# Kernel tuning notes

Measured on AMD Instinct MI355X. Metric: run time of the kernel, lower is better.

Reference implementation:

```python
import jax, jax.numpy as jnp
import numpy as np

# ---- dims ----
V, VR, E, H, NF = 100000, 5000, 300, 256, 150
H2 = 2 * H  # 512


def _lstm_dir(x, Wih, Whh, b, h0, c0):
    # x: (T, B, E); returns hs (T, B, H), final (h, c)
    def step(carry, xt):
        h, c = carry
        z = xt @ Wih.T + h @ Whh.T + b
        i, f, g, o = jnp.split(z, 4, axis=-1)  # torch gate order i,f,g,o
        c = jax.nn.sigmoid(f) * c + jax.nn.sigmoid(i) * jnp.tanh(g)
        h = jax.nn.sigmoid(o) * jnp.tanh(c)
        return (h, c), h
    (hT, cT), hs = jax.lax.scan(step, (h0, c0), x)
    return hs, hT, cT


def bilstm(x, Wih_f, Whh_f, b_f, Wih_b, Whh_b, b_b, state=None):
    # x: (T, B, E) -> out (T, B, 2H), state tuple
    B = x.shape[1]
    if state is None:
        z = jnp.zeros((B, H), x.dtype)
        state = (z, z, z, z)
    h0f, c0f, h0b, c0b = state
    hs_f, hTf, cTf = _lstm_dir(x, Wih_f, Whh_f, b_f, h0f, c0f)
    hs_b, hTb, cTb = _lstm_dir(x[::-1], Wih_b, Whh_b, b_b, h0b, c0b)
    out = jnp.concatenate([hs_f, hs_b[::-1]], axis=-1)
    return out, (hTf, cTf, hTb, cTb)


def abwim_atten(question_out, word_rel, rela_rel, word_emb, rela_emb,
                Wih_f, Whh_f, b_f, Wih_b, Whh_b, b_b, W):
    # question_out: (B, 2H, Sq); word_rel (B,Sw), rela_rel (B,Sr) int
    rela = rela_emb[rela_rel.T]   # (Sr, B, E)
    word = word_emb[word_rel.T]   # (Sw, B, E)
    word_out, state = bilstm(word, Wih_f, Whh_f, b_f, Wih_b, Whh_b, b_b)
    rela_out, _ = bilstm(rela, Wih_f, Whh_f, b_f, Wih_b, Whh_b, b_b, state)
    relation = jnp.concatenate([rela_out, word_out], axis=0).transpose(1, 0, 2)  # (B, R, 2H)
    energy = jnp.einsum('brh,hk,bks->brs', relation, W, question_out)  # (B, R, Sq)
    B, R, Sq = energy.shape
    scale = 1.0 / np.sqrt(R).astype(np.float32)
    alpha = jax.nn.softmax(energy.reshape(B, R * Sq) * scale, axis=-1).reshape(B, R, Sq)
    # sum_r alpha[b,r,s] * relation[b,r,h] -> (B, 2H, Sq)
    return jnp.einsum('brs,brh->bhs', alpha, relation)


def setup_inputs():
    key = jax.random.key(0)
    ks = jax.random.split(key, 24)
    B, Sq, Sw, Sr = 64, 40, 12, 4
    s_emb, s_lstm, s_w = 0.05, 0.05, 0.04
    inp = {
        'question': jax.random.randint(ks[0], (B, Sq), 0, V),
        'word_relation': jax.random.randint(ks[1], (B, Sw), 0, V),
        'rela_relation': jax.random.randint(ks[2], (B, Sr), 0, VR),
        'word_previous': jax.random.randint(ks[3], (B, Sw), 0, V),
        'rela_previous': jax.random.randint(ks[4], (B, Sr), 0, VR),
        'word_emb': jax.random.normal(ks[5], (V, E), jnp.float32) * s_emb,
        'rela_emb': jax.random.normal(ks[6], (VR, E), jnp.float32) * s_emb,
        'Wih_f': jax.random.normal(ks[7], (4 * H, E), jnp.float32) * s_lstm,
        'Whh_f': jax.random.normal(ks[8], (4 * H, H), jnp.float32) * s_lstm,
        'b_f': jnp.zeros((4 * H,), jnp.float32),
        'Wih_b': jax.random.normal(ks[9], (4 * H, E), jnp.float32) * s_lstm,
        'Whh_b': jax.random.normal(ks[10], (4 * H, H), jnp.float32) * s_lstm,
        'b_b': jnp.zeros((4 * H,), jnp.float32),
        'W': jax.random.normal(ks[11], (H2, H2), jnp.float32) * s_w,
        'cnn1_w': jax.random.normal(ks[12], (NF, 2 * H2, 1), jnp.float32) * s_w,
        'cnn1_b': jnp.zeros((NF,), jnp.float32),
        'cnn2_w': jax.random.normal(ks[13], (NF, 2 * H2, 3), jnp.float32) * s_w,
        'cnn2_b': jnp.zeros((NF,), jnp.float32),
        'cnn3_w': jax.random.normal(ks[14], (NF, 2 * H2, 5), jnp.float32) * s_w,
        'cnn3_b': jnp.zeros((NF,), jnp.float32),
        'lin_w': jax.random.normal(ks[15], (1, NF), jnp.float32) * s_w,
        'lin2_w': jax.random.normal(ks[16], (H2, H2), jnp.float32) * s_w,
        'lin2_b': jnp.zeros((H2,), jnp.float32),
    }
    return inp


def _conv1d(x, w, b):
    # x: (B, C, L), w: (O, C, K)
    y = jax.lax.conv_general_dilated(x, w, (1,), 'VALID',
                                     dimension_numbers=('NCH', 'OIH', 'NCH'))
    return y + b[None, :, None]


def reference(question, word_relation, rela_relation, word_previous, rela_previous,
              word_emb, rela_emb, Wih_f, Whh_f, b_f, Wih_b, Whh_b, b_b, W,
              cnn1_w, cnn1_b, cnn2_w, cnn2_b, cnn3_w, cnn3_b, lin_w, lin2_w, lin2_b):
    lstm_p = (Wih_f, Whh_f, b_f, Wih_b, Whh_b, b_b)
    # question encoder (dropout is identity at eval)
    q = word_emb[question.T]                      # (Sq, B, E)
    q_out, _ = bilstm(q, *lstm_p)                 # (Sq, B, 2H)
    question_out = q_out.transpose(1, 2, 0)       # (B, 2H, Sq)
    # reduce one previous hop
    atten_prev = abwim_atten(question_out, word_previous, rela_previous,
                             word_emb, rela_emb, *lstm_p, W)
    qo = question_out - atten_prev
    qo = qo.transpose(0, 2, 1) @ lin2_w.T + lin2_b   # (B, Sq, 2H)
    question_out = qo.transpose(0, 2, 1)             # (B, 2H, Sq)
    # current relation attention
    atten_relation = abwim_atten(question_out, word_relation, rela_relation,
                                 word_emb, rela_emb, *lstm_p, W)
    M = jnp.concatenate([question_out, atten_relation], axis=1)  # (B, 4H, Sq)
    h1 = jnp.max(jax.nn.relu(_conv1d(M, cnn1_w, cnn1_b)), axis=2)  # (B, NF)
    h2 = jnp.max(jax.nn.relu(_conv1d(M, cnn2_w, cnn2_b)), axis=2)
    h3 = jnp.max(jax.nn.relu(_conv1d(M, cnn3_w, cnn3_b)), axis=2)
    h = jnp.maximum(jnp.maximum(h1, h2), h3)
    score = (h @ lin_w.T).squeeze(-1)  # (B,)
    return score
```

## Files before the change

### kernel.cpp

```cpp
#include <hip/hip_runtime.h>
#include <math.h>

#define NEG_INF (-3.402823466e+38f)

typedef __attribute__((ext_vector_type(8))) short short8;
typedef __attribute__((ext_vector_type(8))) unsigned short ushort8;
typedef __attribute__((ext_vector_type(4))) float f32x4;

constexpr int NTOK = 4608;
constexpr int BH = 64 * 256;

constexpr size_t OFF_WQ    = 0;
constexpr size_t OFF_B2    = OFF_WQ    + 524288;
constexpr size_t OFF_XB3T  = OFF_B2    + 2048;
constexpr size_t OFF_WB3T  = OFF_XB3T  + 983040;
constexpr size_t OFF_L2B3T = OFF_WB3T  + 393216;
constexpr size_t OFF_C1B3T = OFF_L2B3T + 393216;
constexpr size_t OFF_C2B3T = OFF_C1B3T + 294912;
constexpr size_t OFF_C3B3T = OFF_C2B3T + 884736;
constexpr size_t OFF_XHI   = OFF_C3B3T + 1474560;
constexpr size_t OFF_XLO   = OFF_XHI   + 737280;
constexpr size_t OFF_XP    = OFF_XLO   + 737280;
constexpr size_t OFF_HSQ   = OFF_XP    + 9437184;
constexpr size_t OFF_HSWP  = OFF_HSQ   + 1310720;
constexpr size_t OFF_HSRP  = OFF_HSWP  + 393216;
constexpr size_t OFF_HSWR  = OFF_HSRP  + 131072;
constexpr size_t OFF_HSRR  = OFF_HSWR  + 393216;
constexpr size_t OFF_CS    = OFF_HSRR  + 131072;
constexpr size_t OFF_RELP  = OFF_CS    + 163840;
constexpr size_t OFF_RELC  = OFF_RELP  + 524288;
constexpr size_t OFF_RELW  = OFF_RELC  + 524288;
constexpr size_t OFF_EN    = OFF_RELW  + 524288;

__device__ inline unsigned short f2bf(float f) {
  unsigned int u = __float_as_uint(f);
  u += 0x7FFFu + ((u >> 16) & 1u);
  return (unsigned short)(u >> 16);
}
__device__ inline float bf2f(unsigned short h) {
  return __uint_as_float(((unsigned int)h) << 16);
}
__device__ inline short8 mk8(unsigned long long a, unsigned long long b) {
  union { unsigned long long q[2]; short8 s; } u;
  u.q[0] = a; u.q[1] = b; return u.s;
}
#define ALD(p) __hip_atomic_load((p), __ATOMIC_RELAXED, __HIP_MEMORY_SCOPE_AGENT)

__global__ __launch_bounds__(256) void k_prep(
    const float* __restrict__ Whh_f, const float* __restrict__ Whh_b,
    const float* __restrict__ b_f,   const float* __restrict__ b_b,
    const float* __restrict__ Wih_f, const float* __restrict__ Wih_b,
    const float* __restrict__ Wat,   const float* __restrict__ l2w,
    const float* __restrict__ c1w, const float* __restrict__ c2w, const float* __restrict__ c3w,
    unsigned short* __restrict__ WHB, float* __restrict__ B2,
    unsigned short* __restrict__ XB3T, unsigned short* __restrict__ WB3T,
    unsigned short* __restrict__ L2B3T,
    unsigned short* __restrict__ C1B3T, unsigned short* __restrict__ C2B3T,
    unsigned short* __restrict__ C3B3T, int* __restrict__ flags) {
  int idx = blockIdx.x * 256 + threadIdx.x;
  if (idx < 3072)
    __hip_atomic_store(flags + idx * 16, 0, __ATOMIC_RELAXED, __HIP_MEMORY_SCOPE_AGENT);
  if (idx < 1048576) {
    int e = idx & 511;
    int k = e & 255, isLo = e >> 8;
    int row = (idx >> 9) & 63;
    int tile = (idx >> 15) & 15;
    int d = idx >> 19;
    int g = row >> 4, uu = row & 15;
    int u = tile * 16 + uu;
    const float* Wh = d ? Whh_b : Whh_f;
    float w = Wh[(size_t)(g * 256 + u) * 256 + k];
    unsigned short hi = f2bf(w);
    WHB[idx] = isLo ? f2bf(w - bf2f(hi)) : hi;
    return;
  }
  idx -= 1048576;
  if (idx < 2048) { B2[idx] = (idx < 1024) ? b_f[idx] : b_b[idx-1024]; return; }
  idx -= 2048;
  unsigned short* dst; int n, k, K;
  float w;
  if (idx < 655360) {
    n = idx / 320; k = idx % 320; K = 320; dst = XB3T;
    w = (k < 300) ? ((n < 1024) ? Wih_f[(size_t)n*300 + k] : Wih_b[(size_t)(n-1024)*300 + k]) : 0.f;
  } else if ((idx -= 655360) < 262144) {
    n = idx >> 9; k = idx & 511; K = 512; dst = WB3T;
    w = Wat[(size_t)k*512 + n];
  } else if ((idx -= 262144) < 262144) {
    n = idx >> 9; k = idx & 511; K = 512; dst = L2B3T;
    w = l2w[(size_t)n*512 + k];
  } else if ((idx -= 262144) < 196608) {
    n = idx >> 10; k = idx & 1023; K = 1024; dst = C1B3T;
    w = (n < 150) ? c1w[(size_t)n*1024 + k] : 0.f;
  } else if ((idx -= 196608) < 589824) {
    n = idx / 3072; k = idx % 3072; K = 3072; dst = C2B3T;
    int kw = k >> 10, c = k & 1023;
    w = (n < 150) ? c2w[((size_t)n*1024 + c)*3 + kw] : 0.f;
  } else if ((idx -= 589824) < 983040) {
    n = idx / 5120; k = idx % 5120; K = 5120; dst = C3B3T;
    int kw = k >> 10, c = k & 1023;
    w = (n < 150) ? c3w[((size_t)n*1024 + c)*5 + kw] : 0.f;
  } else return;
  unsigned short hi = f2bf(w);
  unsigned short lo = f2bf(w - bf2f(hi));
  size_t base = (size_t)n * (3*K);
  dst[base + k] = hi;
  dst[base + K + k] = lo;
  dst[base + 2*K + k] = hi;
}

__global__ __launch_bounds__(320) void k_gather(
    const int* __restrict__ q,  const int* __restrict__ wr, const int* __restrict__ rr,
    const int* __restrict__ wp, const int* __restrict__ rp,
    const float* __restrict__ we, const float* __restrict__ re,
    unsigned short* __restrict__ Xhi, unsigned short* __restrict__ Xlo) {
  int m = blockIdx.x, k = threadIdx.x;
  const float* emb; int row;
  if (m < 2560)      { int t=m>>6,    b=m&63; row = q [b*40+t]; emb = we; }
  else if (m < 3328) { int mm=m-2560; int t=mm>>6,b=mm&63; row = wp[b*12+t]; emb = we; }
  else if (m < 3584) { int mm=m-3328; int t=mm>>6,b=mm&63; row = rp[b*4 +t]; emb = re; }
  else if (m < 4352) { int mm=m-3584; int t=mm>>6,b=mm&63; row = wr[b*12+t]; emb = we; }
  else               { int mm=m-4352; int t=mm>>6,b=mm&63; row = rr[b*4 +t]; emb = re; }
  float v = (k < 300) ? emb[(size_t)row*300 + k] : 0.f;
  unsigned short hi = f2bf(v);
  Xhi[(size_t)m*320 + k] = hi;
  Xlo[(size_t)m*320 + k] = f2bf(v - bf2f(hi));
}

template<bool BIAS>
__global__ __launch_bounds__(256) void k_mgemm(
    const unsigned short* __restrict__ Ahi, const unsigned short* __restrict__ Alo, int lda,
    const unsigned short* __restrict__ Bt, const float* __restrict__ bias,
    float* __restrict__ C, int N, int K) {
  __shared__ unsigned short As[64 * 40];
  __shared__ unsigned short Bs[64 * 40];
  int tid = threadIdx.x;
  int wave = tid >> 6, lane = tid & 63;
  int quad = lane >> 4, l16 = lane & 15;
  int m0 = blockIdx.x << 6, n0 = blockIdx.y << 6;
  int K3 = 3 * K;
  int sr = tid >> 2;
  int sc = (tid & 3) << 3;
  f32x4 acc[4] = {};
  for (int k0 = 0; k0 < K3; k0 += 32) {
    int c = (k0 >= K) + (k0 >= 2*K);
    const unsigned short* Asrc = (c == 2) ? Alo : Ahi;
    int kk = k0 - c * K;
    ushort8 av = *(const ushort8*)(Asrc + (size_t)(m0 + sr) * lda + kk + sc);
    ushort8 bv = *(const ushort8*)(Bt + (size_t)(n0 + sr) * K3 + k0 + sc);
    *(ushort8*)&As[sr * 40 + sc] = av;
    *(ushort8*)&Bs[sr * 40 + sc] = bv;
    __syncthreads();
    short8 a  = *(const short8*)&As[(wave*16 + l16) * 40 + quad*8];
    short8 b0 = *(const short8*)&Bs[( 0 + l16) * 40 + quad*8];
    short8 b1 = *(const short8*)&Bs[(16 + l16) * 40 + quad*8];
    short8 b2 = *(const short8*)&Bs[(32 + l16) * 40 + quad*8];
    short8 b3 = *(const short8*)&Bs[(48 + l16) * 40 + quad*8];
    acc[0] = __builtin_amdgcn_mfma_f32_16x16x32_bf16(a, b0, acc[0], 0, 0, 0);
    acc[1] = __builtin_amdgcn_mfma_f32_16x16x32_bf16(a, b1, acc[1], 0, 0, 0);
    acc[2] = __builtin_amdgcn_mfma_f32_16x16x32_bf16(a, b2, acc[2], 0, 0, 0);
    acc[3] = __builtin_amdgcn_mfma_f32_16x16x32_bf16(a, b3, acc[3], 0, 0, 0);
    __syncthreads();
  }
  int row0 = m0 + wave * 16 + quad * 4;
#pragma unroll
  for (int t = 0; t < 4; t++) {
    int col = n0 + t * 16 + l16;
    float bb = BIAS ? bias[col] : 0.f;
#pragma unroll
    for (int r = 0; r < 4; r++)
      C[(size_t)(row0 + r) * N + col] = acc[t][r] + bb;
  }
}

__global__ __launch_bounds__(256) void k_cgemm(
    const unsigned short* __restrict__ Ahi, const unsigned short* __restrict__ Alo,
    const unsigned short* __restrict__ B1, const unsigned short* __restrict__ B2c,
    const unsigned short* __restrict__ B3,
    float* __restrict__ Y1, float* __restrict__ Y2, float* __restrict__ Y3) {
  __shared__ unsigned short As[64 * 40];
  __shared__ unsigned short Bs[64 * 40];
  int z = blockIdx.z;
  const unsigned short* Bt; float* Y; int K, sidx, chunk;
  if (z < 4)       { Bt = B1;  Y = Y1; K = 1024; sidx = z;      chunk = 768;  }
  else if (z < 12) { Bt = B2c; Y = Y2; K = 3072; sidx = z - 4;  chunk = 1152; }
  else             { Bt = B3;  Y = Y3; K = 5120; sidx = z - 12; chunk = 1920; }
  int K3 = 3 * K;
  int ks = sidx * chunk, ke = ks + chunk;
  int tid = threadIdx.x;
  int wave = tid >> 6, lane = tid & 63;
  int quad = lane >> 4, l16 = lane & 15;
  int m0 = blockIdx.x << 6, n0 = blockIdx.y << 6;
  int sr = tid >> 2;
  int sc = (tid & 3) << 3;
  f32x4 acc[4] = {};
  for (int k0 = ks; k0 < ke; k0 += 32) {
    int c = (k0 >= K) + (k0 >= 2*K);
    const unsigned short* Asrc = (c == 2) ? Alo : Ahi;
    int kk = k0 - c * K;
    ushort8 av = *(const ushort8*)(Asrc + (size_t)(m0 + sr) * 1024 + kk + sc);
    ushort8 bv = *(const ushort8*)(Bt + (size_t)(n0 + sr) * K3 + k0 + sc);
    *(ushort8*)&As[sr * 40 + sc] = av;
    *(ushort8*)&Bs[sr * 40 + sc] = bv;
    __syncthreads();
    short8 a  = *(const short8*)&As[(wave*16 + l16) * 40 + quad*8];
    short8 b0 = *(const short8*)&Bs[( 0 + l16) * 40 + quad*8];
    short8 b1 = *(const short8*)&Bs[(16 + l16) * 40 + quad*8];
    short8 b2 = *(const short8*)&Bs[(32 + l16) * 40 + quad*8];
    short8 b3 = *(const short8*)&Bs[(48 + l16) * 40 + quad*8];
    acc[0] = __builtin_amdgcn_mfma_f32_16x16x32_bf16(a, b0, acc[0], 0, 0, 0);
    acc[1] = __builtin_amdgcn_mfma_f32_16x16x32_bf16(a, b1, acc[1], 0, 0, 0);
    acc[2] = __builtin_amdgcn_mfma_f32_16x16x32_bf16(a, b2, acc[2], 0, 0, 0);
    acc[3] = __builtin_amdgcn_mfma_f32_16x16x32_bf16(a, b3, acc[3], 0, 0, 0);
    __syncthreads();
  }
  int row0 = m0 + wave * 16 + quad * 4;
#pragma unroll
  for (int t = 0; t < 4; t++) {
    int col = n0 + t * 16 + l16;
#pragma unroll
    for (int r = 0; r < 4; r++)
      atomicAdd(&Y[(size_t)(row0 + r) * 192 + col], acc[t][r]);
  }
}

__global__ __launch_bounds__(256) void k_zero(float* __restrict__ p, int n4) {
  int idx = blockIdx.x * 256 + threadIdx.x;
  if (idx < n4) *(float4*)(p + (size_t)idx * 4) = make_float4(0.f, 0.f, 0.f, 0.f);
}

__global__ __launch_bounds__(256, 1) void k_steps(
    const unsigned short* __restrict__ WHB, const float* __restrict__ XP,
    float* __restrict__ hsQ, float* __restrict__ hsWp, float* __restrict__ hsRp,
    float* __restrict__ hsWr, float* __restrict__ hsRr,
    unsigned short* __restrict__ Hhi, unsigned short* __restrict__ Hlo,
    int* __restrict__ flags) {
  int bid = blockIdx.x;
  int chain = bid & 7;
  if (chain >= 6) return;
  int tile = bid >> 3;
  int dir = chain & 1, fam = chain >> 1;
  int tid = threadIdx.x;
  int wave = tid >> 6, lane = tid & 63;
  int quad = lane >> 4, l16 = lane & 15;
  int u0 = tile << 4;

  const unsigned short* wsrc = WHB + (((size_t)dir * 16 + tile) << 15);
  short8 Bh[4][8], Bl[4][8];
#pragma unroll
  for (int nf = 0; nf < 4; nf++)
#pragma unroll
    for (int j = 0; j < 8; j++) {
      const unsigned short* wr = wsrc + (nf * 16 + l16) * 512 + j * 32 + quad * 8;
      Bh[nf][j] = *(const short8*)(wr);
      Bl[nf][j] = *(const short8*)(wr + 256);
    }

  int nsteps = (fam == 0) ? 40 : 16;
  float creg[4] = {0.f, 0.f, 0.f, 0.f};
  int row64 = (wave * 16 + l16) * 64 + quad * 2;

  for (int cs = 0; cs < nsteps; cs++) {
    int t, T, seg; float* hsb;
    if (fam == 0)     { t = cs;      T = 40; seg = 0;                         hsb = hsQ + (size_t)dir * 40 * BH; }
    else if (cs < 12) { t = cs;      T = 12; seg = (fam == 1) ? 2560 : 3584;  hsb = ((fam == 1) ? hsWp : hsWr) + (size_t)dir * 12 * BH; }
    else              { t = cs - 12; T = 4;  seg = (fam == 1) ? 3328 : 4352;  hsb = ((fam == 1) ? hsRp : hsRr) + (size_t)dir * 4 * BH; }
    int t_in = dir ? (T - 1 - t) : t;
    int u = u0 + l16;
    const float* xb = XP + (size_t)(seg + t_in * 64) * 2048 + dir * 1024 + u;
    float xi[4], xf[4], xg[4], xo[4];
#pragma unroll
    for (int r = 0; r < 4; r++) {
      const float* xr = xb + (size_t)(wave * 16 + quad * 4 + r) * 2048;
      xi[r] = xr[0]; xf[r] = xr[256]; xg[r] = xr[512]; xo[r] = xr[768];
    }

    f32x4 acc[4] = {};
    if (cs > 0) {
      if (tid < 16) {
        const int* fp = flags + ((((chain << 1) | ((cs - 1) & 1)) * 16 + tid) << 4);
        while (__hip_atomic_load(fp, __ATOMIC_RELAXED, __HIP_MEMORY_SCOPE_AGENT) < cs)
          __builtin_amdgcn_s_sleep(2);
      }
      __syncthreads();
      size_t slotq = (size_t)(chain * 2 + ((cs - 1) & 1)) * 4096;
      const unsigned long long* ph = (const unsigned long long*)Hhi + slotq + row64;
      const unsigned long long* pl = (const unsigned long long*)Hlo + slotq + row64;
      unsigned long long rv[32];
#pragma unroll
      for (int j = 0; j < 8; j++) { rv[2*j] = ALD(ph + 8*j); rv[2*j+1] = ALD(ph + 8*j + 1); }
#pragma unroll
      for (int j = 0; j < 8; j++) { rv[16+2*j] = ALD(pl + 8*j); rv[16+2*j+1] = ALD(pl + 8*j + 1); }
      short8 ah[8], al[8];
#pragma unroll
      for (int j = 0; j < 8; j++) { ah[j] = mk8(rv[2*j], rv[2*j+1]); al[j] = mk8(rv[16+2*j], rv[16+2*j+1]); }
#pragma unroll
      for (int j = 0; j < 8; j++) {
        acc[0] = __builtin_amdgcn_mfma_f32_16x16x32_bf16(ah[j], Bh[0][j], acc[0], 0, 0, 0);
        acc[1] = __builtin_amdgcn_mfma_f32_16x16x32_bf16(ah[j], Bh[1][j], acc[1], 0, 0, 0);
        acc[2] = __builtin_amdgcn_mfma_f32_16x16x32_bf16(ah[j], Bh[2][j], acc[2], 0, 0, 0);
        acc[3] = __builtin_amdgcn_mfma_f32_16x16x32_bf16(ah[j], Bh[3][j], acc[3], 0, 0, 0);
      }
#pragma unroll
      for (int j = 0; j < 8; j++) {
        acc[0] = __builtin_amdgcn_mfma_f32_16x16x32_bf16(ah[j], Bl[0][j], acc[0], 0, 0, 0);
        acc[1] = __builtin_amdgcn_mfma_f32_16x16x32_bf16(ah[j], Bl[1][j], acc[1], 0, 0, 0);
        acc[2] = __builtin_amdgcn_mfma_f32_16x16x32_bf16(ah[j], Bl[2][j], acc[2], 0, 0, 0);
        acc[3] = __builtin_amdgcn_mfma_f32_16x16x32_bf16(ah[j], Bl[3][j], acc[3], 0, 0, 0);
      }
#pragma unroll
      for (int j = 0; j < 8; j++) {
        acc[0] = __builtin_amdgcn_mfma_f32_16x16x32_bf16(al[j], Bh[0][j], acc[0], 0, 0, 0);
        acc[1] = __builtin_amdgcn_mfma_f32_16x16x32_bf16(al[j], Bh[1][j], acc[1], 0, 0, 0);
        acc[2] = __builtin_amdgcn_mfma_f32_16x16x32_bf16(al[j], Bh[2][j], acc[2], 0, 0, 0);
        acc[3] = __builtin_amdgcn_mfma_f32_16x16x32_bf16(al[j], Bh[3][j], acc[3], 0, 0, 0);
      }
    }
    float hnv[4];
#pragma unroll
    for (int r = 0; r < 4; r++) {
      float zi = acc[0][r] + xi[r];
      float zf = acc[1][r] + xf[r];
      float zg = acc[2][r] + xg[r];
      float zo = acc[3][r] + xo[r];
      float gi = 1.f / (1.f + expf(-zi));
      float gf = 1.f / (1.f + expf(-zf));
      float go = 1.f / (1.f + expf(-zo));
      float gg = tanhf(zg);
      float cn = gf * creg[r] + gi * gg;
      hnv[r] = go * tanhf(cn);
      creg[r] = cn;
    }
    size_t oslot = (size_t)(chain * 2 + (cs & 1)) << 14;
    unsigned short* oh = Hhi + oslot;
    unsigned short* ol = Hlo + oslot;
#pragma unroll
    for (int r = 0; r < 4; r++) {
      int b = wave * 16 + quad * 4 + r;
      unsigned short h16 = f2bf(hnv[r]);
      unsigned short l16v = f2bf(hnv[r] - bf2f(h16));
      unsigned int pk = (unsigned int)h16 | ((unsigned int)l16v << 16);
      unsigned int pw = (unsigned int)__shfl_xor((int)pk, 1, 64);
      if ((lane & 1) == 0) {
        unsigned int hw = (pk & 0xFFFFu) | (pw << 16);
        unsigned int lw = (pk >> 16) | (pw & 0xFFFF0000u);
        __hip_atomic_store((unsigned int*)(oh + b * 256 + u), hw,
                           __ATOMIC_RELAXED, __HIP_MEMORY_SCOPE_AGENT);
        __hip_atomic_store((unsigned int*)(ol + b * 256 + u), lw,
                           __ATOMIC_RELAXED, __HIP_MEMORY_SCOPE_AGENT);
      }
    }
    float* hout = hsb + (size_t)t * BH + u;
#pragma unroll
    for (int r = 0; r < 4; r++) {
      int b = wave * 16 + quad * 4 + r;
      hout[(size_t)b * 256] = hnv[r];
    }
    if (cs + 1 < nsteps) {
      __syncthreads();
      if (tid == 0)
        __hip_atomic_store(flags + ((((chain << 1) | (cs & 1)) * 16 + tile) << 4), cs + 1,
                           __ATOMIC_RELAXED, __HIP_MEMORY_SCOPE_AGENT);
    }
  }
}

__global__ __launch_bounds__(256) void k_qo1(const float* __restrict__ hsQ, float* __restrict__ QT) {
  int idx = blockIdx.x * 256 + threadIdx.x;
  if (idx >= 64*40*512) return;
  int h = idx & 511; int t2 = idx >> 9; int s = t2 % 40; int b = t2 / 40;
  float v;
  if (h < 256) v = hsQ[(size_t)s * BH + b*256 + h];
  else         v = hsQ[(size_t)40 * BH + (size_t)(39 - s) * BH + b*256 + (h - 256)];
  QT[idx] = v;
}

__global__ __launch_bounds__(256) void k_rel(
    const float* __restrict__ hsWp, const float* __restrict__ hsRp,
    const float* __restrict__ hsWr, const float* __restrict__ hsRr,
    float* __restrict__ RELP, float* __restrict__ RELC,
    unsigned short* __restrict__ RPhi, unsigned short* __restrict__ RPlo,
    unsigned short* __restrict__ RChi, unsigned short* __restrict__ RClo) {
  int idx0 = blockIdx.x * 256 + threadIdx.x;
  if (idx0 >= 2*64*16*512) return;
  int call = idx0 >= 64*16*512;
  int idx = idx0 - call * 64*16*512;
  int h = idx & 511; int t2 = idx >> 9; int r = t2 & 15; int b = t2 >> 4;
  const float* hsW = call ? hsWr : hsWp;
  const float* hsR = call ? hsRr : hsRp;
  float v;
  if (r < 4) {
    if (h < 256) v = hsR[(size_t)r * BH + b*256 + h];
    else         v = hsR[(size_t)4 * BH + (size_t)(3 - r) * BH + b*256 + (h - 256)];
  } else {
    int t = r - 4;
    if (h < 256) v = hsW[(size_t)t * BH + b*256 + h];
    else         v = hsW[(size_t)12 * BH + (size_t)(11 - t) * BH + b*256 + (h - 256)];
  }
  unsigned short hi = f2bf(v);
  unsigned short lo = f2bf(v - bf2f(hi));
  if (call) { RELC[idx] = v; RChi[idx] = hi; RClo[idx] = lo; }
  else      { RELP[idx] = v; RPhi[idx] = hi; RPlo[idx] = lo; }
}

__global__ __launch_bounds__(256) void k_energy(
    const float* __restrict__ relW, const float* __restrict__ QT, float* __restrict__ EN) {
  int idx = blockIdx.x * 256 + threadIdx.x;
  if (idx >= 64*16*40) return;
  int s = idx % 40; int t = idx / 40; int r = t & 15; int b = t >> 4;
  const float* rw = relW + (size_t)(b*16 + r) * 512;
  const float* qv = QT   + (size_t)(b*40 + s) * 512;
  float acc = 0.f;
#pragma unroll 4
  for (int k = 0; k < 512; k += 4) {
    float4 a = *(const float4*)(rw + k);
    float4 c = *(const float4*)(qv + k);
    acc += a.x*c.x + a.y*c.y + a.z*c.z + a.w*c.w;
  }
  EN[idx] = acc;
}

__global__ __launch_bounds__(256) void k_softmax(float* __restrict__ EN) {
  int b = blockIdx.x; int tid = threadIdx.x;
  float* e = EN + b * 640;
  float v0 = e[tid] * 0.25f, v1 = e[tid + 256] * 0.25f;
  float v2 = (tid < 128) ? e[tid + 512] * 0.25f : NEG_INF;
  __shared__ float sh[256];
  sh[tid] = fmaxf(v0, fmaxf(v1, v2));
  __syncthreads();
  for (int st = 128; st > 0; st >>= 1) { if (tid < st) sh[tid] = fmaxf(sh[tid], sh[tid+st]); __syncthreads(); }
  float m = sh[0];
  __syncthreads();
  float e0 = expf(v0 - m), e1 = expf(v1 - m);
  float e2 = (tid < 128) ? expf(v2 - m) : 0.f;
  sh[tid] = e0 + e1 + e2;
  __syncthreads();
  for (int st = 128; st > 0; st >>= 1) { if (tid < st) sh[tid] += sh[tid+st]; __syncthreads(); }
  float inv = 1.f / sh[0];
  e[tid] = e0 * inv; e[tid + 256] = e1 * inv;
  if (tid < 128) e[tid + 512] = e2 * inv;
}

__global__ __launch_bounds__(256) void k_atten(
    const float* __restrict__ AL, const float* __restrict__ REL, float* __restrict__ ATT) {
  int idx = blockIdx.x * 256 + threadIdx.x;
  if (idx >= 64*40*512) return;
  int h = idx & 511; int t2 = idx >> 9; int s = t2 % 40; int b = t2 / 40;
  const float* al = AL + b * 640 + s;
  const float* rl = REL + (size_t)b * 16 * 512 + h;
  float acc = 0.f;
#pragma unroll
  for (int r = 0; r < 16; r++) acc += al[r*40] * rl[r*512];
  ATT[idx] = acc;
}

__global__ __launch_bounds__(256) void k_sub(
    const float* __restrict__ QT, const float* __restrict__ ATT,
    unsigned short* __restrict__ Dhi, unsigned short* __restrict__ Dlo) {
  int idx = blockIdx.x * 256 + threadIdx.x;
  if (idx >= 64*40*512) return;
  float v = QT[idx] - ATT[idx];
  unsigned short hi = f2bf(v);
  Dhi[idx] = hi; Dlo[idx] = f2bf(v - bf2f(hi));
}

__global__ __launch_bounds__(256) void k_m2(
    const float* __restrict__ QO2, const float* __restrict__ ATT,
    unsigned short* __restrict__ M2hi, unsigned short* __restrict__ M2lo) {
  int idx = blockIdx.x * 256 + threadIdx.x;
  if (idx >= 2626048) return;
  float v = 0.f;
  if (idx < 2621440) {
    int c = idx & 1023; int m = idx >> 10;
    v = (c < 512) ? QO2[(size_t)m*512 + c] : ATT[(size_t)m*512 + (c - 512)];
  }
  unsigned short hi = f2bf(v);
  M2hi[idx] = hi; M2lo[idx] = f2bf(v - bf2f(hi));
}

__global__ __launch_bounds__(256) void k_pool(
    const float* __restrict__ Y1, const float* __restrict__ Y2, const float* __restrict__ Y3,
    const float* __restrict__ b1, const float* __restrict__ b2, const float* __restrict__ b3,
    const float* __restrict__ lw, float* __restrict__ out) {
  int b = blockIdx.x, o = threadIdx.x;
  float hv = 0.f;
  if (o < 150) {
    const float* y1 = Y1 + (size_t)b*40*192 + o;
    const float* y2 = Y2 + (size_t)b*40*192 + o;
    const float* y3 = Y3 + (size_t)b*40*192 + o;
    float m1 = NEG_INF, m2 = NEG_INF, m3 = NEG_INF;
#pragma unroll 4
    for (int l = 0; l < 40; l++) m1 = fmaxf(m1, y1[l*192]);
#pragma unroll 2
    for (int l = 0; l < 38; l++) m2 = fmaxf(m2, y2[l*192]);
#pragma unroll 2
    for (int l = 0; l < 36; l++) m3 = fmaxf(m3, y3[l*192]);
    float h = fmaxf(fmaxf(m1 + b1[o], m2 + b2[o]), m3 + b3[o]);
    hv = fmaxf(h, 0.f) * lw[o];
  }
  __shared__ float sh[256];
  sh[threadIdx.x] = hv;
  __syncthreads();
  for (int st = 128; st > 0; st >>= 1) { if (threadIdx.x < st) sh[threadIdx.x] += sh[threadIdx.x+st]; __syncthreads(); }
  if (threadIdx.x == 0) out[b] = sh[0];
}

extern "C" void kernel_launch(void* const* d_in, const int* in_sizes, int n_in,
                              void* d_out, int out_size, void* d_ws, size_t ws_size,
                              hipStream_t stream) {
  const int*   q    = (const int*)d_in[0];
  const int*   wrel = (const int*)d_in[1];
  const int*   rrel = (const int*)d_in[2];
  const int*   wprv = (const int*)d_in[3];
  const int*   rprv = (const int*)d_in[4];
  const float* we   = (const float*)d_in[5];
  const float* re   = (const float*)d_in[6];
  const float* Wih_f= (const float*)d_in[7];
  const float* Whh_f= (const float*)d_in[8];
  const float* b_f  = (const float*)d_in[9];
  const float* Wih_b= (const float*)d_in[10];
  const float* Whh_b= (const float*)d_in[11];
  const float* b_b  = (const float*)d_in[12];
  const float* W    = (const float*)d_in[13];
  const float* c1w  = (const float*)d_in[14];
  const float* c1b  = (const float*)d_in[15];
  const float* c2w  = (const float*)d_in[16];
  const float* c2b  = (const float*)d_in[17];
  const float* c3w  = (const float*)d_in[18];
  const float* c3b  = (const float*)d_in[19];
  const float* lw   = (const float*)d_in[20];
  const float* l2w  = (const float*)d_in[21];
  const float* l2b  = (const float*)d_in[22];
  float* out = (float*)d_out;
  float* ws  = (float*)d_ws;

  unsigned short* WHB = (unsigned short*)(ws + OFF_WQ);
  float* B2   = ws + OFF_B2;
  unsigned short* XB3T  = (unsigned short*)(ws + OFF_XB3T);
  unsigned short* WB3T  = (unsigned short*)(ws + OFF_WB3T);
  unsigned short* L2B3T = (unsigned short*)(ws + OFF_L2B3T);
  unsigned short* C1B3T = (unsigned short*)(ws + OFF_C1B3T);
  unsigned short* C2B3T = (unsigned short*)(ws + OFF_C2B3T);
  unsigned short* C3B3T = (unsigned short*)(ws + OFF_C3B3T);
  unsigned short* Xhi   = (unsigned short*)(ws + OFF_XHI);
  unsigned short* Xlo   = (unsigned short*)(ws + OFF_XLO);
  float* XP   = ws + OFF_XP;
  float* HSQ  = ws + OFF_HSQ;
  float* HSWP = ws + OFF_HSWP;
  float* HSRP = ws + OFF_HSRP;
  float* HSWR = ws + OFF_HSWR;
  float* HSRR = ws + OFF_HSRR;
  int*   flags = (int*)(ws + OFF_CS);
  float* RELP = ws + OFF_RELP;
  float* RELC = ws + OFF_RELC;
  float* RELW = ws + OFF_RELW;
  float* EN   = ws + OFF_EN;
  unsigned short* Hhi = (unsigned short*)(ws + OFF_RELP);
  unsigned short* Hlo = Hhi + 196608;
  float* QO1  = XP;
  float* ATT  = XP + 1310720;
  float* QO2  = XP + 2621440;
  unsigned short* Dhi  = (unsigned short*)(XP + 3932160);
  unsigned short* Dlo  = (unsigned short*)(XP + 4587520);
  unsigned short* RPhi = (unsigned short*)(XP + 5242880);
  unsigned short* RPlo = (unsigned short*)(XP + 5505024);
  unsigned short* RChi = (unsigned short*)(XP + 5767168);
  unsigned short* RClo = (unsigned short*)(XP + 6029312);
  unsigned short* M2hi = (unsigned short*)(XP + 5242880);
  unsigned short* M2lo = (unsigned short*)(XP + 6555904);
  float* Y1   = XP + 7868928;
  float* Y2   = XP + 8360448;
  float* Y3   = XP + 8851968;

  k_prep<<<15624, 256, 0, stream>>>(Whh_f, Whh_b, b_f, b_b, Wih_f, Wih_b, W, l2w,
                                    c1w, c2w, c3w,
                                    WHB, B2, XB3T, WB3T, L2B3T, C1B3T, C2B3T, C3B3T, flags);
  k_gather<<<NTOK, 320, 0, stream>>>(q, wrel, rrel, wprv, rprv, we, re, Xhi, Xlo);
  { dim3 g(72, 32); k_mgemm<true><<<g, 256, 0, stream>>>(Xhi, Xlo, 320, XB3T, B2, XP, 2048, 320); }

  k_steps<<<128, 256, 0, stream>>>(WHB, XP, HSQ, HSWP, HSRP, HSWR, HSRR, Hhi, Hlo, flags);

  k_qo1<<<5120, 256, 0, stream>>>(HSQ, QO1);
  k_rel<<<4096, 256, 0, stream>>>(HSWP, HSRP, HSWR, HSRR, RELP, RELC, RPhi, RPlo, RChi, RClo);

  { dim3 g(16, 8); k_mgemm<false><<<g, 256, 0, stream>>>(RPhi, RPlo, 512, WB3T, nullptr, RELW, 512, 512); }
  k_energy<<<160, 256, 0, stream>>>(RELW, QO1, EN);
  k_softmax<<<64, 256, 0, stream>>>(EN);
  k_atten<<<5120, 256, 0, stream>>>(EN, RELP, ATT);
  k_sub<<<5120, 256, 0, stream>>>(QO1, ATT, Dhi, Dlo);
  { dim3 g(40, 8); k_mgemm<true><<<g, 256, 0, stream>>>(Dhi, Dlo, 512, L2B3T, l2b, QO2, 512, 512); }

  { dim3 g(16, 8); k_mgemm<false><<<g, 256, 0, stream>>>(RChi, RClo, 512, WB3T, nullptr, RELW, 512, 512); }
  k_energy<<<160, 256, 0, stream>>>(RELW, QO2, EN);
  k_softmax<<<64, 256, 0, stream>>>(EN);
  k_atten<<<5120, 256, 0, stream>>>(EN, RELC, ATT);

  k_m2<<<10258, 256, 0, stream>>>(QO2, ATT, M2hi, M2lo);
  k_zero<<<1440, 256, 0, stream>>>(Y1, 368640);
  { dim3 g(40, 3, 20); k_cgemm<<<g, 256, 0, stream>>>(M2hi, M2lo, C1B3T, C2B3T, C3B3T, Y1, Y2, Y3); }
  k_pool<<<64, 256, 0, stream>>>(Y1, Y2, Y3, c1b, c2b, c3b, lw, out);
}
```

Before: 785.1 us.

## Use per-step H exchange slots and XCD-aware non-atomic fast path in recurrent kernel

```diff
diff --git a/kernel.cpp b/kernel.cpp
--- a/kernel.cpp
+++ b/kernel.cpp
@@ -45,6 +45,7 @@
   u.q[0] = a; u.q[1] = b; return u.s;
 }
 #define ALD(p) __hip_atomic_load((p), __ATOMIC_RELAXED, __HIP_MEMORY_SCOPE_AGENT)
+#define AST(p, v) __hip_atomic_store((p), (v), __ATOMIC_RELAXED, __HIP_MEMORY_SCOPE_AGENT)
 
 __global__ __launch_bounds__(256) void k_prep(
     const float* __restrict__ Whh_f, const float* __restrict__ Whh_b,
@@ -59,7 +60,9 @@
     unsigned short* __restrict__ C3B3T, int* __restrict__ flags) {
   int idx = blockIdx.x * 256 + threadIdx.x;
   if (idx < 3072)
-    __hip_atomic_store(flags + idx * 16, 0, __ATOMIC_RELAXED, __HIP_MEMORY_SCOPE_AGENT);
+    AST(flags + idx * 16, 0);
+  else if (idx < 3200)
+    AST(flags + 49152 + (idx - 3072) * 16, 0);
   if (idx < 1048576) {
     int e = idx & 511;
     int k = e & 255, isLo = e >> 8;
@@ -232,8 +235,8 @@
     const unsigned short* __restrict__ WHB, const float* __restrict__ XP,
     float* __restrict__ hsQ, float* __restrict__ hsWp, float* __restrict__ hsRp,
     float* __restrict__ hsWr, float* __restrict__ hsRr,
-    unsigned short* __restrict__ Hhi, unsigned short* __restrict__ Hlo,
-    int* __restrict__ flags) {
+    unsigned short* HxA, unsigned short* HxB,
+    int* flags, int* det) {
   int bid = blockIdx.x;
   int chain = bid & 7;
   if (chain >= 6) return;
@@ -244,6 +247,10 @@
   int quad = lane >> 4, l16 = lane & 15;
   int u0 = tile << 4;
 
+  unsigned myxcd;
+  asm volatile("s_getreg_b32 %0, hwreg(HW_REG_XCC_ID)" : "=s"(myxcd));
+  if (tid == 0) AST(det + bid * 16, (int)myxcd + 1);
+
   const unsigned short* wsrc = WHB + (((size_t)dir * 16 + tile) << 15);
   short8 Bh[4][8], Bl[4][8];
 #pragma unroll
@@ -255,9 +262,29 @@
       Bl[nf][j] = *(const short8*)(wr + 256);
     }
 
+  __shared__ int s_fast;
+  int idv = 0;
+  if (tid < 16) {
+    const int* dp = det + (tid * 8 + chain) * 16;
+    int v;
+    while ((v = ALD(dp)) == 0) __builtin_amdgcn_s_sleep(1);
+    idv = v;
+  }
+  if (wave == 0) {
+    int ref = __shfl(idv, 0, 64);
+    unsigned long long bad = __ballot((lane < 16) && (idv != ref));
+    if (lane == 0) s_fast = (bad == 0ULL);
+  }
+  __syncthreads();
+  int fast = s_fast;
+
   int nsteps = (fam == 0) ? 40 : 16;
+  int slot0 = (chain < 2) ? chain * 40 : 80 + (chain - 2) * 16;
   float creg[4] = {0.f, 0.f, 0.f, 0.f};
-  int row64 = (wave * 16 + l16) * 64 + quad * 2;
+  int roff = (quad * 64 + wave * 16 + l16) * 8;
+  int wj = tile >> 1;
+  int wq = ((tile & 1) << 1) + (l16 >> 3);
+  int wbase = ((wj * 4 + wq) * 64) * 4 + ((l16 & 7) >> 1);
 
   for (int cs = 0; cs < nsteps; cs++) {
     int t, T, seg; float* hsb;
@@ -276,23 +303,33 @@
 
     f32x4 acc[4] = {};
     if (cs > 0) {
+      int rs = slot0 + cs - 1;
+      const unsigned short* Hb = (rs < 96) ? (HxA + (size_t)rs * 32768)
+                                           : (HxB + (size_t)(rs - 96) * 32768);
       if (tid < 16) {
-        const int* fp = flags + ((((chain << 1) | ((cs - 1) & 1)) * 16 + tid) << 4);
-        while (__hip_atomic_load(fp, __ATOMIC_RELAXED, __HIP_MEMORY_SCOPE_AGENT) < cs)
-          __builtin_amdgcn_s_sleep(2);
+        const int* fp = flags + ((rs * 16 + tid) << 4);
+        while (ALD(fp) == 0) __builtin_amdgcn_s_sleep(1);
       }
       __syncthreads();
-      size_t slotq = (size_t)(chain * 2 + ((cs - 1) & 1)) * 4096;
-      const unsigned long long* ph = (const unsigned long long*)Hhi + slotq + row64;
-      const unsigned long long* pl = (const unsigned long long*)Hlo + slotq + row64;
-      unsigned long long rv[32];
-#pragma unroll
-      for (int j = 0; j < 8; j++) { rv[2*j] = ALD(ph + 8*j); rv[2*j+1] = ALD(ph + 8*j + 1); }
-#pragma unroll
-      for (int j = 0; j < 8; j++) { rv[16+2*j] = ALD(pl + 8*j); rv[16+2*j+1] = ALD(pl + 8*j + 1); }
       short8 ah[8], al[8];
-#pragma unroll
-      for (int j = 0; j < 8; j++) { ah[j] = mk8(rv[2*j], rv[2*j+1]); al[j] = mk8(rv[16+2*j], rv[16+2*j+1]); }
+      if (fast) {
+#pragma unroll
+        for (int j = 0; j < 8; j++) {
+          ah[j] = *(const short8*)(Hb + j * 2048 + roff);
+          al[j] = *(const short8*)(Hb + 16384 + j * 2048 + roff);
+        }
+      } else {
+        const unsigned long long* ph = (const unsigned long long*)Hb;
+        const unsigned long long* pl = ph + 4096;
+        int r4 = roff >> 2;
+        unsigned long long rv[32];
+#pragma unroll
+        for (int j = 0; j < 8; j++) { rv[2*j] = ALD(ph + j*512 + r4); rv[2*j+1] = ALD(ph + j*512 + r4 + 1); }
+#pragma unroll
+        for (int j = 0; j < 8; j++) { rv[16+2*j] = ALD(pl + j*512 + r4); rv[16+2*j+1] = ALD(pl + j*512 + r4 + 1); }
+#pragma unroll
+        for (int j = 0; j < 8; j++) { ah[j] = mk8(rv[2*j], rv[2*j+1]); al[j] = mk8(rv[16+2*j], rv[16+2*j+1]); }
+      }
 #pragma unroll
       for (int j = 0; j < 8; j++) {
         acc[0] = __builtin_amdgcn_mfma_f32_16x16x32_bf16(ah[j], Bh[0][j], acc[0], 0, 0, 0);
@@ -330,36 +367,35 @@
       hnv[r] = go * tanhf(cn);
       creg[r] = cn;
     }
-    size_t oslot = (size_t)(chain * 2 + (cs & 1)) << 14;
-    unsigned short* oh = Hhi + oslot;
-    unsigned short* ol = Hlo + oslot;
-#pragma unroll
-    for (int r = 0; r < 4; r++) {
-      int b = wave * 16 + quad * 4 + r;
-      unsigned short h16 = f2bf(hnv[r]);
-      unsigned short l16v = f2bf(hnv[r] - bf2f(h16));
-      unsigned int pk = (unsigned int)h16 | ((unsigned int)l16v << 16);
-      unsigned int pw = (unsigned int)__shfl_xor((int)pk, 1, 64);
-      if ((lane & 1) == 0) {
-        unsigned int hw = (pk & 0xFFFFu) | (pw << 16);
-        unsigned int lw = (pk >> 16) | (pw & 0xFFFF0000u);
-        __hip_atomic_store((unsigned int*)(oh + b * 256 + u), hw,
-                           __ATOMIC_RELAXED, __HIP_MEMORY_SCOPE_AGENT);
-        __hip_atomic_store((unsigned int*)(ol + b * 256 + u), lw,
-                           __ATOMIC_RELAXED, __HIP_MEMORY_SCOPE_AGENT);
+    int wslot = slot0 + cs;
+    if (cs + 1 < nsteps) {
+      unsigned short* Ho = (wslot < 96) ? (HxA + (size_t)wslot * 32768)
+                                        : (HxB + (size_t)(wslot - 96) * 32768);
+      unsigned int* ohw = (unsigned int*)Ho + wbase;
+      unsigned int* olw = (unsigned int*)(Ho + 16384) + wbase;
+#pragma unroll
+      for (int r = 0; r < 4; r++) {
+        int b = wave * 16 + quad * 4 + r;
+        unsigned short h16 = f2bf(hnv[r]);
+        unsigned short l16v = f2bf(hnv[r] - bf2f(h16));
+        unsigned int pk = (unsigned int)h16 | ((unsigned int)l16v << 16);
+        unsigned int pw = (unsigned int)__shfl_xor((int)pk, 1, 64);
+        if ((lane & 1) == 0) {
+          unsigned int hw = (pk & 0xFFFFu) | (pw << 16);
+          unsigned int lw = (pk >> 16) | (pw & 0xFFFF0000u);
+          if (fast) { ohw[b * 4] = hw; olw[b * 4] = lw; }
+          else      { AST(ohw + b * 4, hw); AST(olw + b * 4, lw); }
+        }
       }
+      __syncthreads();
+      if (tid == 0)
+        AST(flags + ((wslot * 16 + tile) << 4), 1);
     }
     float* hout = hsb + (size_t)t * BH + u;
 #pragma unroll
     for (int r = 0; r < 4; r++) {
       int b = wave * 16 + quad * 4 + r;
       hout[(size_t)b * 256] = hnv[r];
-    }
-    if (cs + 1 < nsteps) {
-      __syncthreads();
-      if (tid == 0)
-        __hip_atomic_store(flags + ((((chain << 1) | (cs & 1)) * 16 + tile) << 4), cs + 1,
-                           __ATOMIC_RELAXED, __HIP_MEMORY_SCOPE_AGENT);
     }
   }
 }
@@ -550,12 +586,13 @@
   float* HSWR = ws + OFF_HSWR;
   float* HSRR = ws + OFF_HSRR;
   int*   flags = (int*)(ws + OFF_CS);
+  int*   det   = flags + 49152;
   float* RELP = ws + OFF_RELP;
   float* RELC = ws + OFF_RELC;
   float* RELW = ws + OFF_RELW;
   float* EN   = ws + OFF_EN;
-  unsigned short* Hhi = (unsigned short*)(ws + OFF_RELP);
-  unsigned short* Hlo = Hhi + 196608;
+  unsigned short* HxA = (unsigned short*)(ws + OFF_RELP);
+  unsigned short* HxB = (unsigned short*)(ws + OFF_XB3T);
   float* QO1  = XP;
   float* ATT  = XP + 1310720;
   float* QO2  = XP + 2621440;
@@ -577,7 +614,7 @@
   k_gather<<<NTOK, 320, 0, stream>>>(q, wrel, rrel, wprv, rprv, we, re, Xhi, Xlo);
   { dim3 g(72, 32); k_mgemm<true><<<g, 256, 0, stream>>>(Xhi, Xlo, 320, XB3T, B2, XP, 2048, 320); }
 
-  k_steps<<<128, 256, 0, stream>>>(WHB, XP, HSQ, HSWP, HSRP, HSWR, HSRR, Hhi, Hlo, flags);
+  k_steps<<<128, 256, 0, stream>>>(WHB, XP, HSQ, HSWP, HSRP, HSWR, HSRR, HxA, HxB, flags, det);
 
   k_qo1<<<5120, 256, 0, stream>>>(HSQ, QO1);
   k_rel<<<4096, 256, 0, stream>>>(HSWP, HSRP, HSWR, HSRR, RELP, RELC, RPhi, RPlo, RChi, RClo);
```

New measurement: 687.8 us. 1.14x faster.
